# Kernel tuning notes

Hardware: AMD Instinct MI355X
Metric: run time of the kernel (lower is better)

Reference implementation:

```python
import jax, jax.numpy as jnp
import numpy as np

NUM_EXPERTS = 8
HIDDEN = 2048
EXPERT_DIM = 4096
R = 64
LORA_ALPHA = 16
SCALING = LORA_ALPHA / R
TOKENS_PER_EXPERT = 1024


def setup_inputs() -> dict:
    key = jax.random.key(0)
    ks = jax.random.split(key, 7)
    s = lambda shape: 1.0 / np.sqrt(shape[-1])
    return {
        "hidden_states": jax.random.normal(ks[0], (NUM_EXPERTS * TOKENS_PER_EXPERT, HIDDEN), jnp.float32),
        "W_gu": jax.random.normal(ks[1], (2 * EXPERT_DIM, HIDDEN), jnp.float32) * s((HIDDEN,)),
        "A_gu": jax.random.normal(ks[2], (R, HIDDEN), jnp.float32) * s((HIDDEN,)),
        "B_gu": jax.random.normal(ks[3], (2 * EXPERT_DIM, R), jnp.float32) * 0.01,
        "W_d": jax.random.normal(ks[4], (HIDDEN, EXPERT_DIM), jnp.float32) * s((EXPERT_DIM,)),
        "A_d": jax.random.normal(ks[5], (R, EXPERT_DIM), jnp.float32) * s((EXPERT_DIM,)),
        "B_d": jax.random.normal(ks[6], (HIDDEN, R), jnp.float32) * 0.01,
    }


def _lora_linear(x, W, A, B):
    # y = x @ W^T + scaling * (x @ A^T) @ B^T   (nn.Linear convention, no dropout)
    return x @ W.T + (x @ A.T) @ B.T * SCALING


def reference(hidden_states, W_gu, A_gu, B_gu, W_d, A_d, B_d):
    # (E, N, H)
    x = hidden_states.reshape(NUM_EXPERTS, -1, HIDDEN)
    gate_up = _lora_linear(x, W_gu, A_gu, B_gu)          # (E, N, 2*D)
    gate, up = jnp.split(gate_up, 2, axis=-1)             # each (E, N, D)
    h = up * jax.nn.silu(gate)                            # SwiGLU
    out = _lora_linear(h, W_d, A_d, B_d)                  # (E, N, H)
    return out.reshape(-1, HIDDEN)
```

## Files before the change

kernel.cpp:

```cpp
#include <hip/hip_runtime.h>
#include <stdint.h>

typedef __bf16 bf16_t;
typedef __bf16 bf16x8 __attribute__((ext_vector_type(8)));
typedef __bf16 bf16x4 __attribute__((ext_vector_type(4)));
typedef float f32x4 __attribute__((ext_vector_type(4)));

#define GLOAD16(gp, lp)                                                        \
    __builtin_amdgcn_global_load_lds(                                          \
        (const __attribute__((address_space(1))) void*)(gp),                   \
        (__attribute__((address_space(3))) void*)(lp), 16, 0, 0)

#define MFMA16(a, b, c) __builtin_amdgcn_mfma_f32_16x16x32_bf16(a, b, c, 0, 0, 0)

#define SB() __builtin_amdgcn_sched_barrier(0)
#define BAR() asm volatile("s_barrier" ::: "memory")
#define LGKM0() asm volatile("s_waitcnt lgkmcnt(0)" ::: "memory")
#define VMW(n) asm volatile("s_waitcnt vmcnt(" #n ")" ::: "memory")

#define PH_PRE()                                                               \
    do {                                                                       \
        SB();                                                                  \
        BAR();                                                                 \
        LGKM0();                                                               \
        SB();                                                                  \
        __builtin_amdgcn_s_setprio(1);                                         \
    } while (0)
#define PH_POST()                                                              \
    do {                                                                       \
        __builtin_amdgcn_s_setprio(0);                                         \
        SB();                                                                  \
        BAR();                                                                 \
    } while (0)


__global__ __launch_bounds__(256) void cvt_all_kernel(
    const float* __restrict__ x, const float* __restrict__ Wgu,
    const float* __restrict__ Bgu, const float* __restrict__ Wd,
    const float* __restrict__ Bd, const float* __restrict__ Agu,
    const float* __restrict__ Ad, bf16_t* __restrict__ X1,
    bf16_t* __restrict__ W1, bf16_t* __restrict__ W2,
    bf16_t* __restrict__ Abf, bf16_t* __restrict__ Adbf) {
    int b = blockIdx.x;
    const float* src;
    bf16_t* dst;
    int cshift, cmask, ldd, coff, lb;
    if (b < 16384) {
        src = x; dst = X1; cshift = 11; cmask = 2047; ldd = 2112; coff = 0; lb = b;
    } else if (b < 32768) {
        src = Wgu; dst = W1; cshift = 11; cmask = 2047; ldd = 2112; coff = 0; lb = b - 16384;
    } else if (b < 33280) {
        src = Bgu; dst = W1; cshift = 6; cmask = 63; ldd = 2112; coff = 2048; lb = b - 32768;
    } else if (b < 41472) {
        src = Wd; dst = W2; cshift = 12; cmask = 4095; ldd = 4160; coff = 0; lb = b - 33280;
    } else if (b < 41600) {
        src = Bd; dst = W2; cshift = 6; cmask = 63; ldd = 4160; coff = 4096; lb = b - 41472;
    } else if (b < 41728) {
        src = Agu; dst = Abf; cshift = 11; cmask = 2047; ldd = 2048; coff = 0; lb = b - 41600;
    } else {
        src = Ad; dst = Adbf; cshift = 12; cmask = 4095; ldd = 4096; coff = 0; lb = b - 41728;
    }
    int idx = (lb * 256 + threadIdx.x) << 2;
    int r = idx >> cshift;
    int c = idx & cmask;
    float4 v = *(const float4*)(src + idx);
    bf16x4 o = {(bf16_t)v.x, (bf16_t)v.y, (bf16_t)v.z, (bf16_t)v.w};
    *(bf16x4*)(dst + (size_t)r * ldd + coff + c) = o;
}

__global__ __launch_bounds__(256) void lora_kernel(const bf16_t* __restrict__ A,
                                                   int lda,
                                                   const bf16_t* __restrict__ Bw,
                                                   int K, bf16_t* __restrict__ dst,
                                                   int ldd, int coff) {
    __shared__ __align__(16) bf16_t As[64 * 64];
    __shared__ __align__(16) bf16_t Bs[64 * 64];
    const int t = threadIdx.x;
    const int m0 = blockIdx.x * 64;
    const int lane = t & 63, w = t >> 6;
    const int ln15 = lane & 15, q = lane >> 4;

    const int lrow = t >> 3;
    const int lchunk = (t & 7) ^ (lrow & 7);
    const bf16_t* gaL = A + (size_t)(m0 + lrow) * lda + lchunk * 8;
    const bf16_t* gbL = Bw + (size_t)lrow * K + lchunk * 8;
    bf16_t* lA = As + t * 8;
    bf16_t* lB = Bs + t * 8;

    const f32x4 z = {0.f, 0.f, 0.f, 0.f};
    f32x4 acc[4];
#pragma unroll
    for (int j = 0; j < 4; ++j) acc[j] = z;

    int aoffs[2], boffs[2][4];
#pragma unroll
    for (int s = 0; s < 2; ++s) {
        int rowa = w * 16 + ln15;
        aoffs[s] = rowa * 64 + (((q + 4 * s) ^ (rowa & 7)) << 3);
#pragma unroll
        for (int j = 0; j < 4; ++j) {
            int rowb = j * 16 + ln15;
            boffs[s][j] = rowb * 64 + (((q + 4 * s) ^ (rowb & 7)) << 3);
        }
    }

    for (int kt = 0; kt < K; kt += 64) {
        GLOAD16(gaL, lA);
        GLOAD16(gaL + (size_t)32 * lda, lA + 32 * 64);
        GLOAD16(gbL, lB);
        GLOAD16(gbL + (size_t)32 * K, lB + 32 * 64);
        __syncthreads();
#pragma unroll
        for (int s = 0; s < 2; ++s) {
            bf16x8 av = *(const bf16x8*)(As + aoffs[s]);
#pragma unroll
            for (int j = 0; j < 4; ++j) {
                bf16x8 bv = *(const bf16x8*)(Bs + boffs[s][j]);
                acc[j] = MFMA16(av, bv, acc[j]);
            }
        }
        __syncthreads();
        gaL += 64;
        gbL += 64;
    }

#pragma unroll
    for (int j = 0; j < 4; ++j)
#pragma unroll
        for (int rg = 0; rg < 4; ++rg) {
            int m = m0 + w * 16 + q * 4 + rg;
            dst[(size_t)m * ldd + coff + j * 16 + ln15] = (bf16_t)(acc[j][rg] * 0.25f);
        }
}

__global__ __launch_bounds__(256, 2) void gemm1_kernel(const bf16_t* __restrict__ X,
                                                       const bf16_t* __restrict__ Wc,
                                                       bf16_t* __restrict__ X2) {
    constexpr int LDA = 2112, LDW = 2112, LDX2 = 4160, K = 2112;
    __shared__ __align__(16) bf16_t As[256 * 64];
    __shared__ __align__(16) bf16_t Bs[128 * 64];
    const int t = threadIdx.x;
    const int n0 = blockIdx.x * 64;
    const int m0 = blockIdx.y * 256;
    const int lane = t & 63, w = t >> 6, wr = w >> 1, wc = w & 1;
    const int ln15 = lane & 15, q = lane >> 4;

    const int lrow = t >> 3;
    const int lchunk = (t & 7) ^ (lrow & 7);
    const bf16_t* gaL = X + (size_t)(m0 + lrow) * LDA + lchunk * 8;
    const bf16_t* gbgL = Wc + (size_t)(n0 + lrow) * LDW + lchunk * 8;
    const bf16_t* gbuL = Wc + (size_t)(4096 + n0 + lrow) * LDW + lchunk * 8;
    bf16_t* lA = As + t * 8;
    bf16_t* lB = Bs + t * 8;

    const f32x4 z = {0.f, 0.f, 0.f, 0.f};
    f32x4 acc[8][4];
#pragma unroll
    for (int i = 0; i < 8; ++i)
#pragma unroll
        for (int j = 0; j < 4; ++j) acc[i][j] = z;

    const int sw7 = ln15 & 7;
    const int arow = wr * 128 + ln15;
    const int aoff0 = arow * 64 + ((q ^ sw7) << 3);
    const int aoff1 = arow * 64 + (((q + 4) ^ sw7) << 3);
    const int brow = wc * 32 + ln15;
    const int boff0 = brow * 64 + ((q ^ sw7) << 3);
    const int boff1 = brow * 64 + (((q + 4) ^ sw7) << 3);

    for (int kt = 0; kt < K; kt += 64) {
        GLOAD16(gaL, lA);
        GLOAD16(gaL + (size_t)32 * LDA, lA + 32 * 64);
        GLOAD16(gaL + (size_t)64 * LDA, lA + 64 * 64);
        GLOAD16(gaL + (size_t)96 * LDA, lA + 96 * 64);
        GLOAD16(gaL + (size_t)128 * LDA, lA + 128 * 64);
        GLOAD16(gaL + (size_t)160 * LDA, lA + 160 * 64);
        GLOAD16(gaL + (size_t)192 * LDA, lA + 192 * 64);
        GLOAD16(gaL + (size_t)224 * LDA, lA + 224 * 64);
        GLOAD16(gbgL, lB);
        GLOAD16(gbgL + (size_t)32 * LDW, lB + 32 * 64);
        GLOAD16(gbuL, lB + 64 * 64);
        GLOAD16(gbuL + (size_t)32 * LDW, lB + 96 * 64);
        __syncthreads();
#pragma unroll
        for (int s = 0; s < 2; ++s) {
            const int ao = s ? aoff1 : aoff0;
            const int bo = s ? boff1 : boff0;
            bf16x8 bv[4];
            bv[0] = *(const bf16x8*)(Bs + bo);
            bv[1] = *(const bf16x8*)(Bs + bo + 1024);
            bv[2] = *(const bf16x8*)(Bs + bo + 64 * 64);
            bv[3] = *(const bf16x8*)(Bs + bo + 64 * 64 + 1024);
#pragma unroll
            for (int g2 = 0; g2 < 2; ++g2) {
                bf16x8 av[4];
#pragma unroll
                for (int i = 0; i < 4; ++i)
                    av[i] = *(const bf16x8*)(As + ao + (g2 * 4 + i) * 1024);
#pragma unroll
                for (int i = 0; i < 4; ++i)
#pragma unroll
                    for (int j = 0; j < 4; ++j)
                        acc[g2 * 4 + i][j] = MFMA16(av[i], bv[j], acc[g2 * 4 + i][j]);
            }
        }
        __syncthreads();
        gaL += 64;
        gbgL += 64;
        gbuL += 64;
    }

#pragma unroll
    for (int mi = 0; mi < 8; ++mi)
#pragma unroll
        for (int nj = 0; nj < 2; ++nj)
#pragma unroll
            for (int rg = 0; rg < 4; ++rg) {
                int m = m0 + wr * 128 + mi * 16 + q * 4 + rg;
                int d = n0 + wc * 32 + nj * 16 + ln15;
                float g = acc[mi][nj][rg];
                float u = acc[mi][nj + 2][rg];
                float h = u * g / (1.f + __expf(-g));
                X2[(size_t)m * LDX2 + d] = (bf16_t)h;
            }
}

__global__ __launch_bounds__(512, 2) void gemm2_8p_kernel(
    const bf16_t* __restrict__ X2, const bf16_t* __restrict__ Wdc,
    float* __restrict__ out) {
    constexpr int LDA_ = 4160, LDB_ = 4160, NT_ = 65;
    __shared__ __align__(16) bf16_t smem[65536];
    const int t = threadIdx.x;
    const int lane = t & 63, wid = t >> 6;
    const int wr = wid >> 2, wc = wid & 3;
    const int ln15 = lane & 15, q = lane >> 4;
    const int n0 = blockIdx.x * 256;
    const int m0 = blockIdx.y * 256;

    const int sw = ln15 & 7;
    const int offA0 = (wr * 128 + ln15) * 64 + ((q ^ sw) << 3);
    const int offA1 = (wr * 128 + ln15) * 64 + (((q + 4) ^ sw) << 3);
    const int offB0 = (wc * 64 + ln15) * 64 + ((q ^ sw) << 3);
    const int offB1 = (wc * 64 + ln15) * 64 + (((q + 4) ^ sw) << 3);

    const int rr = t >> 3;
    const int lch = (t & 7) ^ (rr & 7);
    const bf16_t* gA = X2 + (size_t)(m0 + rr) * LDA_ + lch * 8;
    const bf16_t* gB0 = Wdc + (size_t)(n0 + rr) * LDB_ + lch * 8;
    const bf16_t* gB2 = Wdc + (size_t)(n0 + 128 + rr) * LDB_ + lch * 8;

    f32x4 acc[8][4];
    const f32x4 z = {0.f, 0.f, 0.f, 0.f};
#pragma unroll
    for (int i = 0; i < 8; ++i)
#pragma unroll
        for (int j = 0; j < 4; ++j) acc[i][j] = z;

    auto stgA0 = [&](int kt, bf16_t* d) {
        GLOAD16(gA + kt, d + t * 8);
        GLOAD16(gA + (size_t)128 * LDA_ + kt, d + 128 * 64 + t * 8);
    };
    auto stgA1 = [&](int kt, bf16_t* d) {
        GLOAD16(gA + (size_t)64 * LDA_ + kt, d + 64 * 64 + t * 8);
        GLOAD16(gA + (size_t)192 * LDA_ + kt, d + 192 * 64 + t * 8);
    };
    auto stgBlo = [&](int kt, bf16_t* d) {
        GLOAD16(gB0 + kt, d + t * 8);
        GLOAD16(gB0 + (size_t)64 * LDB_ + kt, d + 64 * 64 + t * 8);
    };
    auto stgBhi = [&](int kt, bf16_t* d) {
        GLOAD16(gB2 + kt, d + 128 * 64 + t * 8);
        GLOAD16(gB2 + (size_t)64 * LDB_ + kt, d + 192 * 64 + t * 8);
    };

    stgA0(0, smem);
    stgA1(0, smem);
    stgBlo(0, smem + 32768);
    stgBhi(0, smem + 32768);
    stgA0(64, smem + 16384);
    stgBlo(64, smem + 49152);
    stgBhi(64, smem + 49152);
    VMW(6);
    BAR();

    bf16x8 av[4][2], b0[2][2], b1[2][2];
    for (int g = 0; g < NT_; ++g) {
        const int bs = (g & 1) << 14;
        bf16_t* const Asc = smem + bs;
        bf16_t* const Bsc = smem + 32768 + bs;
        bf16_t* const Asn = smem + (bs ^ 16384);
        const int k1 = (g + 1) << 6, k2 = (g + 2) << 6;

#pragma unroll
        for (int m = 0; m < 4; ++m) {
            av[m][0] = *(const bf16x8*)(Asc + offA0 + m * 1024);
            av[m][1] = *(const bf16x8*)(Asc + offA1 + m * 1024);
        }
#pragma unroll
        for (int n = 0; n < 2; ++n) {
            b0[n][0] = *(const bf16x8*)(Bsc + offB0 + n * 1024);
            b0[n][1] = *(const bf16x8*)(Bsc + offB1 + n * 1024);
        }
        if (g + 1 < NT_) stgA1(k1, Asn);
        PH_PRE();
#pragma unroll
        for (int m = 0; m < 4; ++m)
#pragma unroll
            for (int n = 0; n < 2; ++n) {
                acc[m][n] = MFMA16(av[m][0], b0[n][0], acc[m][n]);
                acc[m][n] = MFMA16(av[m][1], b0[n][1], acc[m][n]);
            }
        PH_POST();

#pragma unroll
        for (int n = 0; n < 2; ++n) {
            b1[n][0] = *(const bf16x8*)(Bsc + offB0 + (2 + n) * 1024);
            b1[n][1] = *(const bf16x8*)(Bsc + offB1 + (2 + n) * 1024);
        }
        if (g + 2 < NT_) stgA0(k2, Asc);
        PH_PRE();
#pragma unroll
        for (int m = 0; m < 4; ++m)
#pragma unroll
            for (int n = 0; n < 2; ++n) {
                acc[m][2 + n] = MFMA16(av[m][0], b1[n][0], acc[m][2 + n]);
                acc[m][2 + n] = MFMA16(av[m][1], b1[n][1], acc[m][2 + n]);
            }
        PH_POST();

#pragma unroll
        for (int m = 0; m < 4; ++m) {
            av[m][0] = *(const bf16x8*)(Asc + offA0 + (4 + m) * 1024);
            av[m][1] = *(const bf16x8*)(Asc + offA1 + (4 + m) * 1024);
        }
        if (g + 2 < NT_) stgBlo(k2, Bsc);
        PH_PRE();
#pragma unroll
        for (int m = 0; m < 4; ++m)
#pragma unroll
            for (int n = 0; n < 2; ++n) {
                acc[4 + m][2 + n] = MFMA16(av[m][0], b1[n][0], acc[4 + m][2 + n]);
                acc[4 + m][2 + n] = MFMA16(av[m][1], b1[n][1], acc[4 + m][2 + n]);
            }
        PH_POST();

        if (g + 2 < NT_) stgBhi(k2, Bsc);
        PH_PRE();
#pragma unroll
        for (int m = 0; m < 4; ++m)
#pragma unroll
            for (int n = 0; n < 2; ++n) {
                acc[4 + m][n] = MFMA16(av[m][0], b0[n][0], acc[4 + m][n]);
                acc[4 + m][n] = MFMA16(av[m][1], b0[n][1], acc[4 + m][n]);
            }
        __builtin_amdgcn_s_setprio(0);
        SB();
        if (g + 2 < NT_)
            VMW(6);
        else
            VMW(0);
        BAR();
    }

#pragma unroll
    for (int mi = 0; mi < 8; ++mi)
#pragma unroll
        for (int nj = 0; nj < 4; ++nj)
#pragma unroll
            for (int rg = 0; rg < 4; ++rg) {
                int row = wr * 128 + mi * 16 + q * 4 + rg;
                int col = wc * 64 + nj * 16 + ln15;
                out[(size_t)(m0 + row) * 2048 + (n0 + col)] = acc[mi][nj][rg];
            }
}

extern "C" void kernel_launch(void* const* d_in, const int* in_sizes, int n_in,
                              void* d_out, int out_size, void* d_ws, size_t ws_size,
                              hipStream_t stream) {
    const float* x = (const float*)d_in[0];
    const float* Wgu = (const float*)d_in[1];
    const float* Agu = (const float*)d_in[2];
    const float* Bgu = (const float*)d_in[3];
    const float* Wd = (const float*)d_in[4];
    const float* Ad = (const float*)d_in[5];
    const float* Bd = (const float*)d_in[6];
    float* out = (float*)d_out;

    char* ws = (char*)d_ws;
    bf16_t* X1 = (bf16_t*)(ws);
    bf16_t* W1 = (bf16_t*)(ws + 34603008);
    bf16_t* X2 = (bf16_t*)(ws + 69206016);
    bf16_t* W2 = (bf16_t*)(ws + 137363456);
    bf16_t* Abf = (bf16_t*)(ws + 154402816);
    bf16_t* Adbf = (bf16_t*)(ws + 154664960);

    cvt_all_kernel<<<41984, 256, 0, stream>>>(x, Wgu, Bgu, Wd, Bd, Agu, Ad,
                                              X1, W1, W2, Abf, Adbf);

    lora_kernel<<<128, 256, 0, stream>>>(X1, 2112, Abf, 2048, X1, 2112, 2048);
    gemm1_kernel<<<dim3(64, 32), 256, 0, stream>>>(X1, W1, X2);
    lora_kernel<<<128, 256, 0, stream>>>(X2, 4160, Adbf, 4096, X2, 4160, 4096);
    gemm2_8p_kernel<<<dim3(8, 32), 512, 0, stream>>>(X2, W2, out);
}
```

Baseline: 612.0 us.

## Restructure gemm2 main loop into k-half phases with uniform clamped prefetch

Reorganizes the down-projection GEMM inner loop so that each phase processes one 32-wide k-half across a 4x4 block of MFMA tiles, loading A and B fragments for that half. It replaces the previous quadrant-ordered schedule and conditional tail handling with clamped prefetch addresses, so global-to-LDS loads are issued unconditionally and the wait counts stay uniform. The goal is a more regular load/compute interleave and fewer branches. The cost is redundant loads of the last tile at the end of the loop and a different register-pressure and LDS hazard pattern, which could break correctness if the buffer reuse timing is off.

```diff
diff --git a/kernel.cpp b/kernel.cpp
--- a/kernel.cpp
+++ b/kernel.cpp
@@ -31,6 +31,16 @@
         __builtin_amdgcn_s_setprio(0);                                         \
         SB();                                                                  \
         BAR();                                                                 \
+    } while (0)
+
+#define CL16(aa, bb, mo)                                                       \
+    do {                                                                       \
+        _Pragma("unroll") for (int mi_ = 0; mi_ < 4; ++mi_) {                  \
+            _Pragma("unroll") for (int nj_ = 0; nj_ < 4; ++nj_) {              \
+                acc[(mo) + mi_][nj_] =                                         \
+                    MFMA16(aa[mi_], bb[nj_], acc[(mo) + mi_][nj_]);            \
+            }                                                                  \
+        }                                                                      \
     } while (0)
 
 
@@ -229,6 +239,7 @@
     const bf16_t* __restrict__ X2, const bf16_t* __restrict__ Wdc,
     float* __restrict__ out) {
     constexpr int LDA_ = 4160, LDB_ = 4160, NT_ = 65;
+    constexpr int KLAST = (NT_ - 1) * 64;
     __shared__ __align__(16) bf16_t smem[65536];
     const int t = threadIdx.x;
     const int lane = t & 63, wid = t >> 6;
@@ -273,94 +284,61 @@
         GLOAD16(gB2 + (size_t)64 * LDB_ + kt, d + 192 * 64 + t * 8);
     };
 
+    bf16x8 aL[4], aH[4], bv[4];
+
     stgA0(0, smem);
-    stgA1(0, smem);
     stgBlo(0, smem + 32768);
     stgBhi(0, smem + 32768);
-    stgA0(64, smem + 16384);
-    stgBlo(64, smem + 49152);
-    stgBhi(64, smem + 49152);
-    VMW(6);
+    stgA1(0, smem);
+    stgA0(64 < KLAST ? 64 : KLAST, smem + 16384);
+    VMW(4);
     BAR();
 
-    bf16x8 av[4][2], b0[2][2], b1[2][2];
     for (int g = 0; g < NT_; ++g) {
-        const int bs = (g & 1) << 14;
-        bf16_t* const Asc = smem + bs;
-        bf16_t* const Bsc = smem + 32768 + bs;
-        bf16_t* const Asn = smem + (bs ^ 16384);
-        const int k1 = (g + 1) << 6, k2 = (g + 2) << 6;
-
-#pragma unroll
-        for (int m = 0; m < 4; ++m) {
-            av[m][0] = *(const bf16x8*)(Asc + offA0 + m * 1024);
-            av[m][1] = *(const bf16x8*)(Asc + offA1 + m * 1024);
-        }
-#pragma unroll
-        for (int n = 0; n < 2; ++n) {
-            b0[n][0] = *(const bf16x8*)(Bsc + offB0 + n * 1024);
-            b0[n][1] = *(const bf16x8*)(Bsc + offB1 + n * 1024);
-        }
-        if (g + 1 < NT_) stgA1(k1, Asn);
+        bf16_t* const Asc = smem + ((g & 1) << 14);
+        bf16_t* const Bsc = Asc + 32768;
+        bf16_t* const Asn = smem + (((g & 1) ^ 1) << 14);
+        bf16_t* const Bsn = Asn + 32768;
+        int k1 = (g + 1) << 6;
+        if (k1 > KLAST) k1 = KLAST;
+        int k2 = (g + 2) << 6;
+        if (k2 > KLAST) k2 = KLAST;
+
+#pragma unroll
+        for (int i = 0; i < 4; ++i) aL[i] = *(const bf16x8*)(Asc + offA0 + i * 1024);
+#pragma unroll
+        for (int j = 0; j < 4; ++j) bv[j] = *(const bf16x8*)(Bsc + offB0 + j * 1024);
+        stgBlo(k1, Bsn);
+        VMW(4);
         PH_PRE();
-#pragma unroll
-        for (int m = 0; m < 4; ++m)
-#pragma unroll
-            for (int n = 0; n < 2; ++n) {
-                acc[m][n] = MFMA16(av[m][0], b0[n][0], acc[m][n]);
-                acc[m][n] = MFMA16(av[m][1], b0[n][1], acc[m][n]);
-            }
+        CL16(aL, bv, 0);
         PH_POST();
 
 #pragma unroll
-        for (int n = 0; n < 2; ++n) {
-            b1[n][0] = *(const bf16x8*)(Bsc + offB0 + (2 + n) * 1024);
-            b1[n][1] = *(const bf16x8*)(Bsc + offB1 + (2 + n) * 1024);
-        }
-        if (g + 2 < NT_) stgA0(k2, Asc);
+        for (int i = 0; i < 4; ++i) aH[i] = *(const bf16x8*)(Asc + offA0 + (4 + i) * 1024);
+        stgBhi(k1, Bsn);
         PH_PRE();
-#pragma unroll
-        for (int m = 0; m < 4; ++m)
-#pragma unroll
-            for (int n = 0; n < 2; ++n) {
-                acc[m][2 + n] = MFMA16(av[m][0], b1[n][0], acc[m][2 + n]);
-                acc[m][2 + n] = MFMA16(av[m][1], b1[n][1], acc[m][2 + n]);
-            }
+        CL16(aH, bv, 4);
         PH_POST();
 
 #pragma unroll
-        for (int m = 0; m < 4; ++m) {
-            av[m][0] = *(const bf16x8*)(Asc + offA0 + (4 + m) * 1024);
-            av[m][1] = *(const bf16x8*)(Asc + offA1 + (4 + m) * 1024);
-        }
-        if (g + 2 < NT_) stgBlo(k2, Bsc);
+        for (int i = 0; i < 4; ++i) aL[i] = *(const bf16x8*)(Asc + offA1 + i * 1024);
+#pragma unroll
+        for (int j = 0; j < 4; ++j) bv[j] = *(const bf16x8*)(Bsc + offB1 + j * 1024);
+        stgA1(k1, Asn);
         PH_PRE();
-#pragma unroll
-        for (int m = 0; m < 4; ++m)
-#pragma unroll
-            for (int n = 0; n < 2; ++n) {
-                acc[4 + m][2 + n] = MFMA16(av[m][0], b1[n][0], acc[4 + m][2 + n]);
-                acc[4 + m][2 + n] = MFMA16(av[m][1], b1[n][1], acc[4 + m][2 + n]);
-            }
+        CL16(aL, bv, 0);
         PH_POST();
 
-        if (g + 2 < NT_) stgBhi(k2, Bsc);
+#pragma unroll
+        for (int i = 0; i < 4; ++i) aH[i] = *(const bf16x8*)(Asc + offA1 + (4 + i) * 1024);
+        stgA0(k2, Asc);
+        VMW(4);
         PH_PRE();
-#pragma unroll
-        for (int m = 0; m < 4; ++m)
-#pragma unroll
-            for (int n = 0; n < 2; ++n) {
-                acc[4 + m][n] = MFMA16(av[m][0], b0[n][0], acc[4 + m][n]);
-                acc[4 + m][n] = MFMA16(av[m][1], b0[n][1], acc[4 + m][n]);
-            }
-        __builtin_amdgcn_s_setprio(0);
-        SB();
-        if (g + 2 < NT_)
-            VMW(6);
-        else
-            VMW(0);
-        BAR();
-    }
+        CL16(aH, bv, 4);
+        PH_POST();
+    }
+    VMW(0);
 
 #pragma unroll
     for (int mi = 0; mi < 8; ++mi)
```

Result: no change. 622.0 us (+1.6%).
